# Kernel tuning notes

Measured on AMD Instinct MI355X. Metric: run time of the kernel, lower is better.

The kernel has to match this reference:

```python
import math
import jax, jax.numpy as jnp
import numpy as np

NUM_BUCKETS = 32
MAX_DISTANCE = 128
N_HEADS = 16
D_KV = 64


def _relative_position_bucket(relative_position, num_buckets=NUM_BUCKETS, max_distance=MAX_DISTANCE):
    # bidirectional (encoder) version, faithful to T5Attention._relative_position_bucket
    nb = num_buckets // 2
    rel_buckets = (relative_position > 0).astype(jnp.int32) * nb
    rp = jnp.abs(relative_position)
    max_exact = nb // 2
    is_small = rp < max_exact
    # log-spaced buckets for large distances; clamp arg of log to >=1 to avoid -inf
    rp_large = max_exact + (
        jnp.log(jnp.maximum(rp, 1).astype(jnp.float32) / max_exact)
        / math.log(max_distance / max_exact)
        * (nb - max_exact)
    ).astype(jnp.int32)
    rp_large = jnp.minimum(rp_large, nb - 1)
    return rel_buckets + jnp.where(is_small, rp, rp_large)


def setup_inputs() -> dict:
    key = jax.random.key(0)
    ks = jax.random.split(key, 6)
    B, S, D = 2, 2048, 1024
    scale = 0.02
    return {
        "hidden_states": jax.random.normal(ks[0], (B, S, D), dtype=jnp.float32),
        "Wq": jax.random.normal(ks[1], (D, N_HEADS * D_KV), dtype=jnp.float32) * scale,
        "Wk": jax.random.normal(ks[2], (D, N_HEADS * D_KV), dtype=jnp.float32) * scale,
        "Wv": jax.random.normal(ks[3], (D, N_HEADS * D_KV), dtype=jnp.float32) * scale,
        "Wo": jax.random.normal(ks[4], (N_HEADS * D_KV, D), dtype=jnp.float32) * scale,
        "rel_bias": jax.random.normal(ks[5], (NUM_BUCKETS, N_HEADS), dtype=jnp.float32),
    }


def reference(hidden_states, Wq, Wk, Wv, Wo, rel_bias):
    B, S, D = hidden_states.shape
    H, dk = N_HEADS, D_KV
    q = (hidden_states @ Wq).reshape(B, S, H, dk)
    k = (hidden_states @ Wk).reshape(B, S, H, dk)
    v = (hidden_states @ Wv).reshape(B, S, H, dk)

    pos = jnp.arange(S)
    relative_position = pos[None, :] - pos[:, None]          # [S_q, S_k]
    buckets = _relative_position_bucket(relative_position)    # [S_q, S_k]
    bias = rel_bias[buckets].transpose(2, 0, 1)               # [H, S_q, S_k]

    # T5 attention: NO 1/sqrt(d) scaling
    scores = jnp.einsum('bqhd,bkhd->bhqk', q, k) + bias[None]
    attn = jax.nn.softmax(scores, axis=-1)
    ctx = jnp.einsum('bhqk,bkhd->bqhd', attn, v).reshape(B, S, H * dk)
    return ctx @ Wo
```

## Files before the change

### kernel.cpp

```cpp
#include <hip/hip_runtime.h>
#include <hip/hip_bf16.h>
#include <stdint.h>

#define S_LEN 2048
#define NH 16
#define NB_DELTA (2*S_LEN-1)
#define PST 72
#define LOG2E 1.4426950408889634f

typedef __attribute__((ext_vector_type(8))) __bf16 bf16x8;
typedef __attribute__((ext_vector_type(4))) float f32x4;

__device__ __forceinline__ unsigned short f2bf(float f){
    union { float f; unsigned int u; } v; v.f = f;
    unsigned int u = v.u;
    return (unsigned short)((u + 0x7FFFu + ((u >> 16) & 1u)) >> 16);
}
__device__ __forceinline__ float bf2f(unsigned short u){
    union { unsigned int u; float f; } v; v.u = ((unsigned int)u) << 16;
    return v.f;
}
__device__ __forceinline__ unsigned int pkbf(float a, float b){
    __hip_bfloat162 h = __float22bfloat162_rn(float2{a, b});
    unsigned int u;
    __builtin_memcpy(&u, &h, 4);
    return u;
}
#if __has_builtin(__builtin_amdgcn_exp2f)
__device__ __forceinline__ float fexp2(float x){ return __builtin_amdgcn_exp2f(x); }
#else
__device__ __forceinline__ float fexp2(float x){ return __expf(x * 0.69314718056f); }
#endif

__device__ __forceinline__ void gload16(const void* g, void* l){
    __builtin_amdgcn_global_load_lds(
        (const __attribute__((address_space(1))) void*)(uintptr_t)g,
        (__attribute__((address_space(3))) void*)(uintptr_t)l, 16, 0, 0);
}

__global__ __launch_bounds__(256) void prep_kernel(
    const float* __restrict__ hs, unsigned short* __restrict__ hsb,
    const float* __restrict__ W0, const float* __restrict__ W1,
    const float* __restrict__ W2, const float* __restrict__ W3,
    unsigned short* __restrict__ D0, unsigned short* __restrict__ D1,
    unsigned short* __restrict__ D2, unsigned short* __restrict__ D3,
    const float* __restrict__ rel_bias, float* __restrict__ biasT){
    if (blockIdx.z == 4) {
        int bi = blockIdx.y * 32 + blockIdx.x;
        for (int it = 0; it < 4; it++) {
            int i = bi * 4096 + it * 1024 + threadIdx.x * 4;
            float4 f = *(const float4*)(hs + i);
            ushort4 o;
            o.x = f2bf(f.x); o.y = f2bf(f.y); o.z = f2bf(f.z); o.w = f2bf(f.w);
            *(ushort4*)(hsb + i) = o;
        }
        if (bi < 16) {
            int t = bi * 256 + threadIdx.x;
            if (t < NB_DELTA) {
                int delta = t - (S_LEN - 1);
                int bucket = (delta > 0) ? 16 : 0;
                int a = delta < 0 ? -delta : delta;
                int b;
                if (a < 8) b = a;
                else {
                    int bl = 33 - __builtin_clz(a * a);
                    b = bl < 15 ? bl : 15;
                }
                bucket += b;
                for (int h = 0; h < NH; h++)
                    biasT[h * NB_DELTA + t] = rel_bias[bucket * NH + h];
            }
        }
        return;
    }
    const float* src; unsigned short* dst;
    switch (blockIdx.z) {
        case 0: src = W0; dst = D0; break;
        case 1: src = W1; dst = D1; break;
        case 2: src = W2; dst = D2; break;
        default: src = W3; dst = D3; break;
    }
    __shared__ float tile[32][33];
    int bx = blockIdx.x, by = blockIdx.y;
    int tx = threadIdx.x & 31, ty = threadIdx.x >> 5;
    for (int i = 0; i < 4; i++)
        tile[ty + 8*i][tx] = src[(size_t)(by*32 + ty + 8*i) * 1024 + bx*32 + tx];
    __syncthreads();
    for (int i = 0; i < 4; i++)
        dst[(size_t)(bx*32 + ty + 8*i) * 1024 + by*32 + tx] = f2bf(tile[tx][ty + 8*i]);
}

template<int MODE, int BM>
__global__ __launch_bounds__(256) void gemm_bt_kernel(const unsigned short* __restrict__ A,
                                                      const unsigned short* __restrict__ BT,
                                                      float* __restrict__ C0,
                                                      unsigned short* __restrict__ C1,
                                                      int Kdim, int ldc){
    constexpr int IT = BM / 32;
    __shared__ __align__(16) unsigned short As[BM * 64];
    __shared__ __align__(16) unsigned short Bs[128 * 64];
    const int t = threadIdx.x;
    const int wave = t >> 6, lane = t & 63;
    const int quad = lane >> 4, l16 = lane & 15;
    const int wm = (wave >> 1) * (BM / 2), wn = (wave & 1) * 64;
    const size_t row0 = (size_t)blockIdx.y * BM, col0 = (size_t)blockIdx.x * 128;

    const int srow8 = lane >> 3;
    const int gg = (lane & 7) ^ srow8;
    const unsigned short* gA = A  + (row0 + wave * 8 + srow8) * (size_t)Kdim + gg * 8;
    const unsigned short* gB = BT + (col0 + wave * 8 + srow8) * (size_t)Kdim + gg * 8;

    f32x4 acc[IT][4] = {};

    for (int kt = 0; kt < Kdim; kt += 64) {
        for (int p = 0; p < BM / 32; p++)
            gload16(gA + (size_t)(p * 32) * Kdim + kt, &As[(p * 32 + wave * 8) * 64]);
        for (int p = 0; p < 4; p++)
            gload16(gB + (size_t)(p * 32) * Kdim + kt, &Bs[(p * 32 + wave * 8) * 64]);
        __syncthreads();
        bf16x8 a[2][IT], b[2][4];
        for (int ks = 0; ks < 2; ks++) {
            for (int i = 0; i < IT; i++)
                a[ks][i] = *(const bf16x8*)(&As[(wm + i*16 + l16) * 64 + (((ks*4 + quad) ^ (l16 & 7)) * 8)]);
            for (int j = 0; j < 4; j++)
                b[ks][j] = *(const bf16x8*)(&Bs[(wn + j*16 + l16) * 64 + (((ks*4 + quad) ^ (l16 & 7)) * 8)]);
        }
        for (int ks = 0; ks < 2; ks++)
            for (int i = 0; i < IT; i++)
                for (int j = 0; j < 4; j++)
                    acc[i][j] = __builtin_amdgcn_mfma_f32_16x16x32_bf16(a[ks][i], b[ks][j], acc[i][j], 0, 0, 0);
        __syncthreads();
    }
    for (int i = 0; i < IT; i++)
        for (int j = 0; j < 4; j++) {
            size_t r0 = row0 + wm + i*16 + quad*4;
            size_t c  = col0 + wn + j*16 + l16;
            if (MODE == 0) {
                for (int r = 0; r < 4; r++)
                    C0[(r0 + r) * ldc + c] = acc[i][j][r];
            } else {
                float qs = (c < 1024) ? LOG2E : 1.0f;
                for (int r = 0; r < 4; r++)
                    C1[(r0 + r) * ldc + c] = f2bf(acc[i][j][r] * qs);
            }
        }
}

__global__ __launch_bounds__(256) void vtrans_kernel(const unsigned short* __restrict__ qkv,
                                                     unsigned short* __restrict__ vt){
    __shared__ unsigned short tile[64][72];
    const int v0 = blockIdx.x * 64, s0 = blockIdx.y * 64, b = blockIdx.z;
    const int tx = threadIdx.x & 7, ty = threadIdx.x >> 3;
    for (int i = 0; i < 2; i++)
        *(int4*)&tile[ty + 32*i][tx * 8] =
            *(const int4*)(qkv + (size_t)(b * 2048 + s0 + ty + 32*i) * 3072 + 2048 + v0 + tx * 8);
    __syncthreads();
    for (int i = 0; i < 2; i++) {
        int v = ty + 32*i;
        int sl = tx * 8;
        ushort4 o0, o1;
        o0.x = tile[sl+0][v]; o0.y = tile[sl+1][v]; o0.z = tile[sl+2][v]; o0.w = tile[sl+3][v];
        o1.x = tile[sl+4][v]; o1.y = tile[sl+5][v]; o1.z = tile[sl+6][v]; o1.w = tile[sl+7][v];
        unsigned short* dst = vt + (size_t)(b * 1024 + v0 + v) * 2048 + s0 + sl;
        *(ushort4*)dst = o0; *(ushort4*)(dst + 4) = o1;
    }
}

__global__ __launch_bounds__(256, 4) void flash10_kernel(
    const unsigned short* __restrict__ qkv,
    const unsigned short* __restrict__ vt,
    const float* __restrict__ biasT,
    const float* __restrict__ rel_bias,
    unsigned short* __restrict__ ctxpb,
    float* __restrict__ rsbuf)
{
    const int qt = blockIdx.x, h = blockIdx.y;
    const int b = blockIdx.z >> 1, ck = blockIdx.z & 1;
    const int kt0 = ck << 10;
    const int t = threadIdx.x;
    const int w = t >> 6, lane = t & 63, quad = lane >> 4, l16 = lane & 15;
    const int q0 = qt * 128;

    __shared__ __align__(16) unsigned short Ks[64 * 64];
    __shared__ __align__(16) unsigned short Vs[64 * 64];
    __shared__ __align__(16) unsigned short Pb[128 * PST];
    __shared__ float bias_s[192];

    const float b15 = (rel_bias[15 * NH + h] - 16.f) * LOG2E;
    const float b31 = (rel_bias[31 * NH + h] - 16.f) * LOG2E;

    for (int s = 0; s < 4; s++) {
        int g = t + s * 256;
        int r = g >> 3, c = (g & 7) * 8;
        *(int4*)&Pb[r * PST + c] =
            *(const int4*)(qkv + (size_t)(b * S_LEN + q0 + r) * 3072 + h * 64 + c);
    }
    __syncthreads();
    bf16x8 qb[2][2];
    for (int nt = 0; nt < 2; nt++)
        for (int ks = 0; ks < 2; ks++)
            qb[ks][nt] = *(const bf16x8*)&Pb[(w * 32 + nt * 16 + l16) * PST + ks * 32 + quad * 8];

    float rsum[2] = {0.f, 0.f};
    f32x4 ctx[4][2] = {};

    const float* biasRow = biasT + h * NB_DELTA + 2047;

    const int srow8 = lane >> 3;
    const int gg = (lane & 7) ^ srow8;
    const int swz = ((l16 & 7) * 8);

    for (int kt = kt0; kt < kt0 + 1024; kt += 64) {
        const int off = kt - q0;
        const bool cst = (off >= 255) || (off <= -191);
        __syncthreads();
        {
            const unsigned short* kb = qkv + (size_t)(b * S_LEN + kt + w * 8 + srow8) * 3072 + 1024 + h * 64 + gg * 8;
            const unsigned short* vb = vt + (size_t)(b * 1024 + h * 64 + w * 8 + srow8) * 2048 + kt + gg * 8;
            gload16(kb,                     &Ks[(w * 8) * 64]);
            gload16(kb + (size_t)32 * 3072, &Ks[(32 + w * 8) * 64]);
            gload16(vb,                     &Vs[(w * 8) * 64]);
            gload16(vb + (size_t)32 * 2048, &Vs[(32 + w * 8) * 64]);
            if (!cst && t < 192) bias_s[t] = (biasRow[off - 127 + t] - 16.f) * LOG2E;
        }
        __syncthreads();

        f32x4 st[4][2] = {};
        for (int ks = 0; ks < 2; ks++)
            for (int nb = 0; nb < 4; nb++) {
                bf16x8 ka = *(const bf16x8*)&Ks[(nb * 16 + l16) * 64 + (((ks * 4 + quad) * 8) ^ swz)];
                st[nb][0] = __builtin_amdgcn_mfma_f32_16x16x32_bf16(ka, qb[ks][0], st[nb][0], 0, 0, 0);
                st[nb][1] = __builtin_amdgcn_mfma_f32_16x16x32_bf16(ka, qb[ks][1], st[nb][1], 0, 0, 0);
            }
        const float bc = (off > 0) ? b31 : b15;
        for (int nt = 0; nt < 2; nt++) {
            const int ib = quad * 4 + 127 - w * 32 - nt * 16 - l16;
            float rs = 0.f;
            for (int nb = 0; nb < 4; nb++) {
                float e0, e1, e2, e3;
                if (cst) {
                    e0 = fexp2(st[nb][nt][0] + bc);
                    e1 = fexp2(st[nb][nt][1] + bc);
                    e2 = fexp2(st[nb][nt][2] + bc);
                    e3 = fexp2(st[nb][nt][3] + bc);
                } else {
                    e0 = fexp2(st[nb][nt][0] + bias_s[ib + nb * 16 + 0]);
                    e1 = fexp2(st[nb][nt][1] + bias_s[ib + nb * 16 + 1]);
                    e2 = fexp2(st[nb][nt][2] + bias_s[ib + nb * 16 + 2]);
                    e3 = fexp2(st[nb][nt][3] + bias_s[ib + nb * 16 + 3]);
                }
                rs += (e0 + e1) + (e2 + e3);
                uint2 pk; pk.x = pkbf(e0, e1); pk.y = pkbf(e2, e3);
                *(uint2*)&Pb[(w * 32 + nt * 16 + l16) * PST + nb * 16 + quad * 4] = pk;
            }
            rsum[nt] += rs;
        }
        for (int ks = 0; ks < 2; ks++) {
            bf16x8 pb0 = *(const bf16x8*)&Pb[(w * 32 + l16) * PST + ks * 32 + quad * 8];
            bf16x8 pb1 = *(const bf16x8*)&Pb[(w * 32 + 16 + l16) * PST + ks * 32 + quad * 8];
            for (int nd = 0; nd < 4; nd++) {
                bf16x8 va = *(const bf16x8*)&Vs[(nd * 16 + l16) * 64 + (((ks * 4 + quad) * 8) ^ swz)];
                ctx[nd][0] = __builtin_amdgcn_mfma_f32_16x16x32_bf16(va, pb0, ctx[nd][0], 0, 0, 0);
                ctx[nd][1] = __builtin_amdgcn_mfma_f32_16x16x32_bf16(va, pb1, ctx[nd][1], 0, 0, 0);
            }
        }
    }
    unsigned short* cp = ctxpb + (size_t)ck * 4096 * 1024;
    for (int nt = 0; nt < 2; nt++) {
        float rs = rsum[nt];
        rs += __shfl_xor(rs, 16, 64);
        rs += __shfl_xor(rs, 32, 64);
        int row = b * S_LEN + q0 + w * 32 + nt * 16 + l16;
        if (quad == 0) rsbuf[((size_t)ck * 4096 + row) * 16 + h] = rs;
        for (int nd = 0; nd < 4; nd++) {
            uint2 pk;
            pk.x = pkbf(ctx[nd][nt][0], ctx[nd][nt][1]);
            pk.y = pkbf(ctx[nd][nt][2], ctx[nd][nt][3]);
            *(uint2*)&cp[(size_t)row * 1024 + h * 64 + nd * 16 + quad * 4] = pk;
        }
    }
}

__global__ __launch_bounds__(256) void combine_kernel(const unsigned short* __restrict__ ctxpb,
                                                      const float* __restrict__ rsbuf,
                                                      unsigned short* __restrict__ ctxb){
    int e = blockIdx.x * 256 + threadIdx.x;
    int row = e >> 8;
    int c4 = (e & 255) * 4;
    int h = c4 >> 6;
    float l = rsbuf[(size_t)row * 16 + h] + rsbuf[((size_t)4096 + row) * 16 + h];
    ushort4 a  = *(const ushort4*)&ctxpb[(size_t)row * 1024 + c4];
    ushort4 b2 = *(const ushort4*)&ctxpb[(size_t)4096 * 1024 + (size_t)row * 1024 + c4];
    float inv = 1.f / l;
    uint2 o;
    o.x = pkbf((bf2f(a.x) + bf2f(b2.x)) * inv, (bf2f(a.y) + bf2f(b2.y)) * inv);
    o.y = pkbf((bf2f(a.z) + bf2f(b2.z)) * inv, (bf2f(a.w) + bf2f(b2.w)) * inv);
    *(uint2*)&ctxb[(size_t)row * 1024 + c4] = o;
}

extern "C" void kernel_launch(void* const* d_in, const int* in_sizes, int n_in,
                              void* d_out, int out_size, void* d_ws, size_t ws_size,
                              hipStream_t stream) {
    const float* hs       = (const float*)d_in[0];
    const float* Wq       = (const float*)d_in[1];
    const float* Wk       = (const float*)d_in[2];
    const float* Wv       = (const float*)d_in[3];
    const float* Wo       = (const float*)d_in[4];
    const float* rel_bias = (const float*)d_in[5];
    float* out = (float*)d_out;

    char* ws = (char*)d_ws;
    float* biasT          = (float*)ws;           ws += 262144;
    unsigned short* hsb   = (unsigned short*)ws;  ws += 8388608;
    unsigned short* WT    = (unsigned short*)ws;  ws += 6291456;
    unsigned short* WoT   = (unsigned short*)ws;  ws += 2097152;
    unsigned short* qkvb  = (unsigned short*)ws;  ws += 25165824;
    unsigned short* Vtg   = (unsigned short*)ws;  ws += 8388608;
    unsigned short* ctxb  = (unsigned short*)ws;  ws += 8388608;
    unsigned short* ctxpb = (unsigned short*)ws;  ws += 16777216;
    float* rsbuf          = (float*)ws;

    prep_kernel<<<dim3(32, 32, 5), 256, 0, stream>>>(
        hs, hsb, Wq, Wk, Wv, Wo,
        WT, WT + 1024 * 1024, WT + 2 * 1024 * 1024, WoT, rel_bias, biasT);

    gemm_bt_kernel<1, 64><<<dim3(24, 64), 256, 0, stream>>>(hsb, WT, nullptr, qkvb, 1024, 3072);
    vtrans_kernel<<<dim3(16, 32, 2), 256, 0, stream>>>(qkvb, Vtg);
    flash10_kernel<<<dim3(S_LEN / 128, NH, 4), 256, 0, stream>>>(qkvb, Vtg, biasT, rel_bias, ctxpb, rsbuf);
    combine_kernel<<<4096, 256, 0, stream>>>(ctxpb, rsbuf, ctxb);
    gemm_bt_kernel<0, 64><<<dim3(8, 64), 256, 0, stream>>>(ctxb, WoT, out, nullptr, 1024, 1024);
}
```

Before: 208.1 us.

## Fuse V transpose into QKV GEMM and double-buffer K/V in flash attention

```diff
diff --git a/kernel.cpp b/kernel.cpp
--- a/kernel.cpp
+++ b/kernel.cpp
@@ -68,7 +68,7 @@
                 }
                 bucket += b;
                 for (int h = 0; h < NH; h++)
-                    biasT[h * NB_DELTA + t] = rel_bias[bucket * NH + h];
+                    biasT[h * NB_DELTA + t] = (rel_bias[bucket * NH + h] - 16.f) * LOG2E;
             }
         }
         return;
@@ -95,6 +95,7 @@
                                                       const unsigned short* __restrict__ BT,
                                                       float* __restrict__ C0,
                                                       unsigned short* __restrict__ C1,
+                                                      unsigned short* __restrict__ Vt,
                                                       int Kdim, int ldc){
     constexpr int IT = BM / 32;
     __shared__ __align__(16) unsigned short As[BM * 64];
@@ -138,39 +139,24 @@
             if (MODE == 0) {
                 for (int r = 0; r < 4; r++)
                     C0[(r0 + r) * ldc + c] = acc[i][j][r];
-            } else {
+            } else if (c < 2048) {
                 float qs = (c < 1024) ? LOG2E : 1.0f;
                 for (int r = 0; r < 4; r++)
                     C1[(r0 + r) * ldc + c] = f2bf(acc[i][j][r] * qs);
-            }
-        }
-}
-
-__global__ __launch_bounds__(256) void vtrans_kernel(const unsigned short* __restrict__ qkv,
-                                                     unsigned short* __restrict__ vt){
-    __shared__ unsigned short tile[64][72];
-    const int v0 = blockIdx.x * 64, s0 = blockIdx.y * 64, b = blockIdx.z;
-    const int tx = threadIdx.x & 7, ty = threadIdx.x >> 3;
-    for (int i = 0; i < 2; i++)
-        *(int4*)&tile[ty + 32*i][tx * 8] =
-            *(const int4*)(qkv + (size_t)(b * 2048 + s0 + ty + 32*i) * 3072 + 2048 + v0 + tx * 8);
-    __syncthreads();
-    for (int i = 0; i < 2; i++) {
-        int v = ty + 32*i;
-        int sl = tx * 8;
-        ushort4 o0, o1;
-        o0.x = tile[sl+0][v]; o0.y = tile[sl+1][v]; o0.z = tile[sl+2][v]; o0.w = tile[sl+3][v];
-        o1.x = tile[sl+4][v]; o1.y = tile[sl+5][v]; o1.z = tile[sl+6][v]; o1.w = tile[sl+7][v];
-        unsigned short* dst = vt + (size_t)(b * 1024 + v0 + v) * 2048 + s0 + sl;
-        *(ushort4*)dst = o0; *(ushort4*)(dst + 4) = o1;
-    }
-}
-
-__global__ __launch_bounds__(256, 4) void flash10_kernel(
+            } else {
+                size_t bb = r0 >> 11, s = r0 & 2047;
+                ushort4 o;
+                o.x = f2bf(acc[i][j][0]); o.y = f2bf(acc[i][j][1]);
+                o.z = f2bf(acc[i][j][2]); o.w = f2bf(acc[i][j][3]);
+                *(ushort4*)(Vt + ((bb << 10) + (c - 2048)) * 2048 + s) = o;
+            }
+        }
+}
+
+__global__ __launch_bounds__(512, 4) void flash11_kernel(
     const unsigned short* __restrict__ qkv,
     const unsigned short* __restrict__ vt,
     const float* __restrict__ biasT,
-    const float* __restrict__ rel_bias,
     unsigned short* __restrict__ ctxpb,
     float* __restrict__ rsbuf)
 {
@@ -179,23 +165,32 @@
     const int kt0 = ck << 10;
     const int t = threadIdx.x;
     const int w = t >> 6, lane = t & 63, quad = lane >> 4, l16 = lane & 15;
-    const int q0 = qt * 128;
-
-    __shared__ __align__(16) unsigned short Ks[64 * 64];
-    __shared__ __align__(16) unsigned short Vs[64 * 64];
-    __shared__ __align__(16) unsigned short Pb[128 * PST];
-    __shared__ float bias_s[192];
-
-    const float b15 = (rel_bias[15 * NH + h] - 16.f) * LOG2E;
-    const float b31 = (rel_bias[31 * NH + h] - 16.f) * LOG2E;
+    const int q0 = qt * 256;
+
+    __shared__ __align__(16) unsigned short Ks[2][64 * 64];
+    __shared__ __align__(16) unsigned short Vs[2][64 * 64];
+    __shared__ __align__(16) unsigned short Pb[256 * PST];
+    __shared__ float bias_b[1280];
 
     for (int s = 0; s < 4; s++) {
-        int g = t + s * 256;
+        int g = t + s * 512;
         int r = g >> 3, c = (g & 7) * 8;
         *(int4*)&Pb[r * PST + c] =
             *(const int4*)(qkv + (size_t)(b * S_LEN + q0 + r) * 3072 + h * 64 + c);
     }
+    {
+        const float* bsrc = biasT + h * NB_DELTA + (kt0 - q0 + 1792);
+        for (int u = t; u < 1279; u += 512) bias_b[u] = bsrc[u];
+    }
+    const int srow8 = lane >> 3;
+    const int gg = (lane & 7) ^ srow8;
+    const int swz = (l16 & 7) * 8;
+    const unsigned short* kbase = qkv + (size_t)(b * S_LEN + w * 8 + srow8) * 3072 + 1024 + h * 64 + gg * 8;
+    const unsigned short* vbase = vt + (size_t)(b * 1024 + h * 64 + w * 8 + srow8) * 2048 + gg * 8;
+    gload16(kbase + (size_t)kt0 * 3072, &Ks[0][(w * 8) * 64]);
+    gload16(vbase + kt0,                &Vs[0][(w * 8) * 64]);
     __syncthreads();
+
     bf16x8 qb[2][2];
     for (int nt = 0; nt < 2; nt++)
         for (int ks = 0; ks < 2; ks++)
@@ -203,67 +198,53 @@
 
     float rsum[2] = {0.f, 0.f};
     f32x4 ctx[4][2] = {};
-
-    const float* biasRow = biasT + h * NB_DELTA + 2047;
-
-    const int srow8 = lane >> 3;
-    const int gg = (lane & 7) ^ srow8;
-    const int swz = ((l16 & 7) * 8);
-
-    for (int kt = kt0; kt < kt0 + 1024; kt += 64) {
-        const int off = kt - q0;
-        const bool cst = (off >= 255) || (off <= -191);
-        __syncthreads();
-        {
-            const unsigned short* kb = qkv + (size_t)(b * S_LEN + kt + w * 8 + srow8) * 3072 + 1024 + h * 64 + gg * 8;
-            const unsigned short* vb = vt + (size_t)(b * 1024 + h * 64 + w * 8 + srow8) * 2048 + kt + gg * 8;
-            gload16(kb,                     &Ks[(w * 8) * 64]);
-            gload16(kb + (size_t)32 * 3072, &Ks[(32 + w * 8) * 64]);
-            gload16(vb,                     &Vs[(w * 8) * 64]);
-            gload16(vb + (size_t)32 * 2048, &Vs[(32 + w * 8) * 64]);
-            if (!cst && t < 192) bias_s[t] = (biasRow[off - 127 + t] - 16.f) * LOG2E;
-        }
-        __syncthreads();
-
+    const int ib0 = 255 + quad * 4 - w * 32 - l16;
+
+    int cur = 0;
+    for (int i = 0; i < 16; i++) {
+        if (i < 15) {
+            int ktn = kt0 + (i + 1) * 64;
+            gload16(kbase + (size_t)ktn * 3072, &Ks[cur ^ 1][(w * 8) * 64]);
+            gload16(vbase + ktn,                &Vs[cur ^ 1][(w * 8) * 64]);
+        }
         f32x4 st[4][2] = {};
+        __builtin_amdgcn_s_setprio(1);
         for (int ks = 0; ks < 2; ks++)
             for (int nb = 0; nb < 4; nb++) {
-                bf16x8 ka = *(const bf16x8*)&Ks[(nb * 16 + l16) * 64 + (((ks * 4 + quad) * 8) ^ swz)];
+                bf16x8 ka = *(const bf16x8*)&Ks[cur][(nb * 16 + l16) * 64 + (((ks * 4 + quad) * 8) ^ swz)];
                 st[nb][0] = __builtin_amdgcn_mfma_f32_16x16x32_bf16(ka, qb[ks][0], st[nb][0], 0, 0, 0);
                 st[nb][1] = __builtin_amdgcn_mfma_f32_16x16x32_bf16(ka, qb[ks][1], st[nb][1], 0, 0, 0);
             }
-        const float bc = (off > 0) ? b31 : b15;
+        __builtin_amdgcn_s_setprio(0);
+        const int ibt = ib0 + i * 64;
         for (int nt = 0; nt < 2; nt++) {
-            const int ib = quad * 4 + 127 - w * 32 - nt * 16 - l16;
+            const int ib = ibt - nt * 16;
             float rs = 0.f;
             for (int nb = 0; nb < 4; nb++) {
-                float e0, e1, e2, e3;
-                if (cst) {
-                    e0 = fexp2(st[nb][nt][0] + bc);
-                    e1 = fexp2(st[nb][nt][1] + bc);
-                    e2 = fexp2(st[nb][nt][2] + bc);
-                    e3 = fexp2(st[nb][nt][3] + bc);
-                } else {
-                    e0 = fexp2(st[nb][nt][0] + bias_s[ib + nb * 16 + 0]);
-                    e1 = fexp2(st[nb][nt][1] + bias_s[ib + nb * 16 + 1]);
-                    e2 = fexp2(st[nb][nt][2] + bias_s[ib + nb * 16 + 2]);
-                    e3 = fexp2(st[nb][nt][3] + bias_s[ib + nb * 16 + 3]);
-                }
+                const float* bp = &bias_b[ib + nb * 16];
+                float e0 = fexp2(st[nb][nt][0] + bp[0]);
+                float e1 = fexp2(st[nb][nt][1] + bp[1]);
+                float e2 = fexp2(st[nb][nt][2] + bp[2]);
+                float e3 = fexp2(st[nb][nt][3] + bp[3]);
                 rs += (e0 + e1) + (e2 + e3);
                 uint2 pk; pk.x = pkbf(e0, e1); pk.y = pkbf(e2, e3);
                 *(uint2*)&Pb[(w * 32 + nt * 16 + l16) * PST + nb * 16 + quad * 4] = pk;
             }
             rsum[nt] += rs;
         }
+        __builtin_amdgcn_s_setprio(1);
         for (int ks = 0; ks < 2; ks++) {
             bf16x8 pb0 = *(const bf16x8*)&Pb[(w * 32 + l16) * PST + ks * 32 + quad * 8];
             bf16x8 pb1 = *(const bf16x8*)&Pb[(w * 32 + 16 + l16) * PST + ks * 32 + quad * 8];
             for (int nd = 0; nd < 4; nd++) {
-                bf16x8 va = *(const bf16x8*)&Vs[(nd * 16 + l16) * 64 + (((ks * 4 + quad) * 8) ^ swz)];
+                bf16x8 va = *(const bf16x8*)&Vs[cur][(nd * 16 + l16) * 64 + (((ks * 4 + quad) * 8) ^ swz)];
                 ctx[nd][0] = __builtin_amdgcn_mfma_f32_16x16x32_bf16(va, pb0, ctx[nd][0], 0, 0, 0);
                 ctx[nd][1] = __builtin_amdgcn_mfma_f32_16x16x32_bf16(va, pb1, ctx[nd][1], 0, 0, 0);
             }
         }
+        __builtin_amdgcn_s_setprio(0);
+        __syncthreads();
+        cur ^= 1;
     }
     unsigned short* cp = ctxpb + (size_t)ck * 4096 * 1024;
     for (int nt = 0; nt < 2; nt++) {
@@ -324,9 +305,8 @@
         hs, hsb, Wq, Wk, Wv, Wo,
         WT, WT + 1024 * 1024, WT + 2 * 1024 * 1024, WoT, rel_bias, biasT);
 
-    gemm_bt_kernel<1, 64><<<dim3(24, 64), 256, 0, stream>>>(hsb, WT, nullptr, qkvb, 1024, 3072);
-    vtrans_kernel<<<dim3(16, 32, 2), 256, 0, stream>>>(qkvb, Vtg);
-    flash10_kernel<<<dim3(S_LEN / 128, NH, 4), 256, 0, stream>>>(qkvb, Vtg, biasT, rel_bias, ctxpb, rsbuf);
+    gemm_bt_kernel<1, 64><<<dim3(24, 64), 256, 0, stream>>>(hsb, WT, nullptr, qkvb, Vtg, 1024, 3072);
+    flash11_kernel<<<dim3(S_LEN / 256, NH, 4), 512, 0, stream>>>(qkvb, Vtg, biasT, ctxpb, rsbuf);
     combine_kernel<<<4096, 256, 0, stream>>>(ctxpb, rsbuf, ctxb);
-    gemm_bt_kernel<0, 64><<<dim3(8, 64), 256, 0, stream>>>(ctxb, WoT, out, nullptr, 1024, 1024);
-}
+    gemm_bt_kernel<0, 64><<<dim3(8, 64), 256, 0, stream>>>(ctxb, WoT, out, nullptr, nullptr, 1024, 1024);
+}
```

Measured after the change: 195.0 us. 1.07x faster.
